# Optimization experiments

Hardware: AMD Instinct MI355X
Metric: run time of the kernel (lower is better)

Reference implementation:

```python
import jax, jax.numpy as jnp
import numpy as np

N = 50000        # total nodes
E = 800000       # edges (before self-loops)
G = 512          # graphs in batch
F_IN = 300       # num_node_features
H = 4            # heads
C = 64           # graph_hidden_channels (per head)
HC = H * C       # 256
NHID = 300
NOUT = 512
NEG_SLOPE = 0.2


def setup_inputs() -> dict:
    key = jax.random.key(0)
    ks = jax.random.split(key, 20)
    x = jax.random.normal(ks[0], (N, F_IN), dtype=jnp.float32)
    edge_index = jax.random.randint(ks[1], (2, E), 0, N, dtype=jnp.int32)
    batch = jnp.sort(jax.random.randint(ks[2], (N,), 0, G, dtype=jnp.int32))

    def lin(k, fan_in, shape):
        s = 1.0 / np.sqrt(fan_in)
        return jax.random.uniform(k, shape, jnp.float32, -s, s)

    params = {
        'W1': lin(ks[3], F_IN, (F_IN, HC)), 'a1s': lin(ks[4], C, (H, C)),
        'a1d': lin(ks[5], C, (H, C)), 'b1': jnp.zeros((HC,), jnp.float32),
        'W2': lin(ks[6], HC, (HC, HC)), 'a2s': lin(ks[7], C, (H, C)),
        'a2d': lin(ks[8], C, (H, C)), 'b2': jnp.zeros((HC,), jnp.float32),
        'W3': lin(ks[9], HC, (HC, HC)), 'a3s': lin(ks[10], C, (H, C)),
        'a3d': lin(ks[11], C, (H, C)), 'b3': jnp.zeros((HC,), jnp.float32),
        'Wm1': lin(ks[12], HC, (HC, NHID)), 'bm1': lin(ks[13], HC, (NHID,)),
        'Wm2': lin(ks[14], NHID, (NHID, NOUT)), 'bm2': lin(ks[15], NHID, (NOUT,)),
    }
    return dict(x=x, edge_index=edge_index, batch=batch, **params)


def gat_conv(x, src, dst, W, a_s, a_d, b):
    # x: [N, Fin] -> h: [N, H, C]
    h = (x @ W).reshape(N, H, C)
    al_s = jnp.sum(h * a_s, axis=-1)   # [N, H]
    al_d = jnp.sum(h * a_d, axis=-1)   # [N, H]
    e = jax.nn.leaky_relu(al_s[src] + al_d[dst], NEG_SLOPE)  # [Etot, H]
    # segment softmax over incoming edges per destination node
    m = jax.ops.segment_max(e, dst, num_segments=N)          # [N, H]
    m = jnp.where(jnp.isfinite(m), m, 0.0)
    ex = jnp.exp(e - m[dst])
    s = jax.ops.segment_sum(ex, dst, num_segments=N)
    alpha = ex / (s[dst] + 1e-16)                            # [Etot, H]
    out = jax.ops.segment_sum(alpha[:, :, None] * h[src], dst, num_segments=N)
    return out.reshape(N, HC) + b


def reference(x, edge_index, batch, W1, a1s, a1d, b1, W2, a2s, a2d, b2,
              W3, a3s, a3d, b3, Wm1, bm1, Wm2, bm2):
    loops = jnp.arange(N, dtype=edge_index.dtype)
    src = jnp.concatenate([edge_index[0], loops])
    dst = jnp.concatenate([edge_index[1], loops])

    h = jax.nn.relu(gat_conv(x, src, dst, W1, a1s, a1d, b1))
    h = jax.nn.relu(gat_conv(h, src, dst, W2, a2s, a2d, b2))
    h = gat_conv(h, src, dst, W3, a3s, a3d, b3)

    # global mean pool over graphs
    sums = jax.ops.segment_sum(h, batch, num_segments=G)           # [G, HC]
    cnts = jax.ops.segment_sum(jnp.ones((N,), h.dtype), batch, num_segments=G)
    pooled = sums / jnp.maximum(cnts, 1.0)[:, None]

    z = jax.nn.relu(pooled @ Wm1 + bm1)
    return z @ Wm2 + bm2
```

## Files before the change

### kernel.cpp

```cpp
#include <hip/hip_runtime.h>
#include <hip/hip_fp16.h>
#include <hip/hip_fp8.h>
#include <cstdint>

#define N_NODES 50000
#define M_PAD   50048
#define E_EDGES 800000
#define ETOT (E_EDGES + N_NODES)
#define G_GRAPHS 512
#define FIN 300
#define K1P 320
#define HC 256
#define NHID 300
#define NOUT 512
#define NBLK 196
#define ROWB 391
#define QPX  49

typedef unsigned short u16;
typedef unsigned char  u8;
typedef __attribute__((ext_vector_type(8))) _Float16 f16x8;
typedef __attribute__((ext_vector_type(4))) float f32x4;
typedef __attribute__((ext_vector_type(2))) float f32x2;

__device__ __forceinline__ float leaky(float x){ return x > 0.f ? x : 0.2f * x; }

#if __has_builtin(__builtin_amdgcn_cvt_pk_fp8_f32) && __has_builtin(__builtin_amdgcn_cvt_pk_f32_fp8)
#define FP8_HW 1
#else
#define FP8_HW 0
#endif

__device__ __forceinline__ u8 f2fp8(float v){
#if FP8_HW
    int b = __builtin_amdgcn_cvt_pk_fp8_f32(v, v, 0, false);
    return (u8)(b & 0xff);
#else
    return (u8)__hip_cvt_float_to_fp8(v, __HIP_SATFINITE, __HIP_E4M3);
#endif
}

__device__ __forceinline__ f32x4 fp8x4tof(unsigned u){
#if FP8_HW
    f32x2 lo = __builtin_amdgcn_cvt_pk_f32_fp8(u, false);
    f32x2 hi = __builtin_amdgcn_cvt_pk_f32_fp8(u, true);
    return (f32x4){lo.x, lo.y, hi.x, hi.y};
#else
    auto d1 = [](u8 b)->float{
        __half_raw hr = __hip_cvt_fp8_to_halfraw((__hip_fp8_storage_t)b, __HIP_E4M3);
        return __half2float(*reinterpret_cast<__half*>(&hr));
    };
    return (f32x4){d1((u8)(u & 0xff)), d1((u8)((u >> 8) & 0xff)),
                   d1((u8)((u >> 16) & 0xff)), d1((u8)((u >> 24) & 0xff))};
#endif
}

__device__ __forceinline__ unsigned packh2(float a, float b){
    __half2 h = __floats2half2_rn(a, b);
    return *reinterpret_cast<unsigned*>(&h);
}
__device__ __forceinline__ float2 unpackh2(unsigned u){
    __half2 h = *reinterpret_cast<__half2*>(&u);
    return __half22float2(h);
}

__global__ void zero_i32(int* __restrict__ p, int n){
    int i = blockIdx.x * blockDim.x + threadIdx.x;
    if (i < n) p[i] = 0;
}

__global__ void hist_kernel(const int* __restrict__ ei, int* __restrict__ counts){
    int i = blockIdx.x * blockDim.x + threadIdx.x;
    if (i >= ETOT) return;
    int d = (i < E_EDGES) ? ei[E_EDGES + i] : (i - E_EDGES);
    atomicAdd(&counts[d], 1);
}


__global__ __launch_bounds__(256) void bsum_kernel(const int* __restrict__ counts,
                                                   int* __restrict__ bsum){
    int b = blockIdx.x, t = threadIdx.x;
    int i = b * 256 + t;
    int v = (i < N_NODES) ? counts[i] : 0;
    #pragma unroll
    for (int o = 32; o >= 1; o >>= 1) v += __shfl_xor(v, o, 64);
    __shared__ int ws[4];
    if ((t & 63) == 0) ws[t >> 6] = v;
    __syncthreads();
    if (t == 0) bsum[b] = ws[0] + ws[1] + ws[2] + ws[3];
}

__global__ __launch_bounds__(256) void bscan_kernel(const int* __restrict__ bsum,
                                                    int* __restrict__ boff,
                                                    int* __restrict__ rs){
    int t = threadIdx.x;
    int v = (t < NBLK) ? bsum[t] : 0;
    __shared__ int sd[256];
    sd[t] = v;
    __syncthreads();
    for (int off = 1; off < 256; off <<= 1){
        int u = (t >= off) ? sd[t - off] : 0;
        __syncthreads();
        sd[t] += u;
        __syncthreads();
    }
    if (t < NBLK) boff[t] = sd[t] - v;
    if (t == 0) rs[N_NODES] = ETOT;
}

__global__ __launch_bounds__(256) void offsets_kernel(const int* __restrict__ counts,
                                                      const int* __restrict__ boff,
                                                      int* __restrict__ rs,
                                                      int* __restrict__ cursor){
    int b = blockIdx.x, t = threadIdx.x;
    int i = b * 256 + t;
    int v = (i < N_NODES) ? counts[i] : 0;
    __shared__ int sd[256];
    sd[t] = v;
    __syncthreads();
    for (int off = 1; off < 256; off <<= 1){
        int u = (t >= off) ? sd[t - off] : 0;
        __syncthreads();
        sd[t] += u;
        __syncthreads();
    }
    if (i < N_NODES){
        int o = boff[b] + sd[t] - v;
        rs[i] = o; cursor[i] = o;
    }
}

__global__ void scatter_kernel(const int* __restrict__ ei, int* __restrict__ cursor,
                               int* __restrict__ csr_src){
    int i = blockIdx.x * blockDim.x + threadIdx.x;
    if (i >= ETOT) return;
    int s, d;
    if (i < E_EDGES){ s = ei[i]; d = ei[E_EDGES + i]; }
    else            { s = d = i - E_EDGES; }
    int pos = atomicAdd(&cursor[d], 1);
    csr_src[pos] = s;
}


__global__ void conv_x_kernel(const float* __restrict__ x, __half* __restrict__ xf){
    int row = blockIdx.x, t = threadIdx.x;
    float v = 0.f;
    if (row < N_NODES && t < FIN) v = x[(size_t)row * FIN + t];
    xf[(size_t)row * K1P + t] = __float2half(v);
}

__global__ void conv_w_kernel(const float* __restrict__ W, __half* __restrict__ wf,
                              int K, int Kp){
    int col = blockIdx.x, k = threadIdx.x;
    float v = (k < K) ? W[(size_t)k * HC + col] : 0.f;
    wf[(size_t)col * Kp + k] = __float2half(v);
}

__global__ void pad_h_kernel(__half* __restrict__ hf){
    int row = N_NODES + blockIdx.x;
    int t = threadIdx.x;
    hf[(size_t)row * HC + t] = __float2half(0.f);
}

__global__ __launch_bounds__(256) void gemm_fp16(const __half* __restrict__ A,
                                                 const __half* __restrict__ Bt,
                                                 u8* __restrict__ Cq,
                                                 int Kp, int Mvalid){
    const int wgid = blockIdx.x;
    const int x    = wgid & 7, i = wgid >> 3;
    const int y    = x * QPX + (i >> 1);
    if (y >= ROWB) return;
    const int cx   = i & 1;
    const int col0 = cx * 128;
    const int row0 = y * 128;

    __shared__ u16 smem[16384];
    const int t    = threadIdx.x;
    const int lane = t & 63;
    const int w    = t >> 6;
    const int fr   = lane & 15, fq = lane >> 4;

    const int rA0 = t >> 2, sA0 = t & 3;

    auto aoff = [](int db, int row, int slot)->int{
        return db * 4096 + row * 32 + ((slot ^ ((row >> 1) & 3)) * 8);
    };
    auto boff = [](int db, int row, int slot)->int{
        return 8192 + db * 4096 + row * 32 + ((slot ^ ((row >> 1) & 3)) * 8);
    };

    f32x4 acc[2][8];
    #pragma unroll
    for (int m = 0; m < 2; ++m)
        #pragma unroll
        for (int n = 0; n < 8; ++n) acc[m][n] = (f32x4){0.f, 0.f, 0.f, 0.f};

    const int nt = Kp >> 5;
    int4 va0, va1, vb0, vb1;

    auto stage_load = [&](int kt){
        const int k0 = kt * 32;
        va0 = *(const int4*)(A  + (size_t)(row0 + rA0)      * Kp + k0 + sA0 * 8);
        va1 = *(const int4*)(A  + (size_t)(row0 + rA0 + 64) * Kp + k0 + sA0 * 8);
        vb0 = *(const int4*)(Bt + (size_t)(col0 + rA0)      * Kp + k0 + sA0 * 8);
        vb1 = *(const int4*)(Bt + (size_t)(col0 + rA0 + 64) * Kp + k0 + sA0 * 8);
    };
    auto stage_write = [&](int db){
        *(int4*)&smem[aoff(db, rA0,      sA0)] = va0;
        *(int4*)&smem[aoff(db, rA0 + 64, sA0)] = va1;
        *(int4*)&smem[boff(db, rA0,      sA0)] = vb0;
        *(int4*)&smem[boff(db, rA0 + 64, sA0)] = vb1;
    };

    stage_load(0); stage_write(0);
    __syncthreads();

    for (int kt = 0; kt < nt; ++kt){
        const int db = kt & 1;
        if (kt + 1 < nt) stage_load(kt + 1);

        f16x8 af[2], bf[8];
        #pragma unroll
        for (int m = 0; m < 2; ++m){
            int row = w * 32 + m * 16 + fr;
            af[m] = *(const f16x8*)&smem[aoff(db, row, fq)];
        }
        #pragma unroll
        for (int n = 0; n < 8; ++n){
            int col = n * 16 + fr;
            bf[n] = *(const f16x8*)&smem[boff(db, col, fq)];
        }
        #pragma unroll
        for (int m = 0; m < 2; ++m)
            #pragma unroll
            for (int n = 0; n < 8; ++n)
                acc[m][n] = __builtin_amdgcn_mfma_f32_16x16x32_f16(af[m], bf[n], acc[m][n], 0, 0, 0);

        if (kt + 1 < nt) stage_write(db ^ 1);
        __syncthreads();
    }

    #pragma unroll
    for (int m = 0; m < 2; ++m){
        int rowb = row0 + w * 32 + m * 16 + fq * 4;
        #pragma unroll
        for (int r = 0; r < 4; ++r){
            int row = rowb + r;
            if (row < Mvalid){
                #pragma unroll
                for (int n = 0; n < 8; ++n)
                    Cq[(size_t)row * HC + col0 + n * 16 + fr] = f2fp8(acc[m][n][r]);
            }
        }
    }
}

__global__ __launch_bounds__(256) void al_kernel(const u8* __restrict__ htq,
                                                 const float* __restrict__ a_s,
                                                 const float* __restrict__ a_d,
                                                 float* __restrict__ als,
                                                 float* __restrict__ ald){
    int wave = threadIdx.x >> 6, lane = threadIdx.x & 63;
    int n = blockIdx.x * 4 + wave;
    if (n >= N_NODES) return;
    const unsigned u = *(const unsigned*)(htq + (size_t)n * HC + 4 * lane);
    f32x4 f = fp8x4tof(u);
    const float4 as4 = *(const float4*)(a_s + 4 * lane);
    const float4 ad4 = *(const float4*)(a_d + 4 * lane);
    float ps = f.x * as4.x + f.y * as4.y + f.z * as4.z + f.w * as4.w;
    float pd = f.x * ad4.x + f.y * ad4.y + f.z * ad4.z + f.w * ad4.w;
    #pragma unroll
    for (int o = 8; o >= 1; o >>= 1){
        ps += __shfl_xor(ps, o, 64);
        pd += __shfl_xor(pd, o, 64);
    }
    if ((lane & 15) == 0){
        als[n * 4 + (lane >> 4)] = ps;
        ald[n * 4 + (lane >> 4)] = pd;
    }
}

__global__ __launch_bounds__(256) void aggregate_kernel(const u8* __restrict__ htq,
                                                        const float* __restrict__ als,
                                                        const float* __restrict__ ald,
                                                        const int* __restrict__ rs,
                                                        const int* __restrict__ csr,
                                                        const float* __restrict__ bias,
                                                        __half* __restrict__ hf,
                                                        int do_relu){
    int wave = threadIdx.x >> 6, lane = threadIdx.x & 63;
    int n = blockIdx.x * 4 + wave;
    if (n >= N_NODES) return;
    const int s0 = rs[n], s1 = rs[n + 1];
    const int deg = s1 - s0;
    const int hsel = lane >> 4;
    const float4 adv = *(const float4*)(ald + (size_t)n * 4);
    const float ad0 = adv.x, ad1 = adv.y, ad2 = adv.z, ad3 = adv.w;

    float4 acc = {0.f, 0.f, 0.f, 0.f};
    float sm0 = 0.f, sm1 = 0.f, sm2 = 0.f, sm3 = 0.f;

    if (deg <= 64){
        const int i = s0 + lane;
        int s = 0;
        float ex0 = 0.f, ex1 = 0.f, ex2 = 0.f, ex3 = 0.f;
        if (i < s1){
            s = csr[i];
            float4 a = *(const float4*)(als + (size_t)s * 4);
            ex0 = __expf(leaky(a.x + ad0));
            ex1 = __expf(leaky(a.y + ad1));
            ex2 = __expf(leaky(a.z + ad2));
            ex3 = __expf(leaky(a.w + ad3));
        }
        sm0 = ex0; sm1 = ex1; sm2 = ex2; sm3 = ex3;
        const unsigned p01 = packh2(ex0, ex1);
        const unsigned p23 = packh2(ex2, ex3);
        const bool loH = (hsel < 2);
        const bool evH = ((hsel & 1) == 0);

        const int dp = (deg + 7) & ~7;
        for (int j = 0; j < dp; j += 8){
            int sj[8]; float aw[8];
            #pragma unroll
            for (int k = 0; k < 8; ++k){
                const int jj = j + k;
                sj[k] = __shfl(s, jj, 64);
                unsigned q01 = __shfl(p01, jj, 64);
                unsigned q23 = __shfl(p23, jj, 64);
                float2 f2 = unpackh2(loH ? q01 : q23);
                aw[k] = evH ? f2.x : f2.y;
            }
            unsigned u[8];
            #pragma unroll
            for (int k = 0; k < 8; ++k)
                u[k] = *(const unsigned*)(htq + (size_t)sj[k] * HC + 4 * lane);
            #pragma unroll
            for (int k = 0; k < 8; ++k){
                f32x4 f = fp8x4tof(u[k]);
                acc.x += aw[k] * f.x; acc.y += aw[k] * f.y;
                acc.z += aw[k] * f.z; acc.w += aw[k] * f.w;
            }
        }
    } else {
        for (int base = s0; base < s1; base += 64){
            const int i = base + lane;
            int s = 0;
            float ex0 = 0.f, ex1 = 0.f, ex2 = 0.f, ex3 = 0.f;
            if (i < s1){
                s = csr[i];
                float4 a = *(const float4*)(als + (size_t)s * 4);
                ex0 = __expf(leaky(a.x + ad0));
                ex1 = __expf(leaky(a.y + ad1));
                ex2 = __expf(leaky(a.z + ad2));
                ex3 = __expf(leaky(a.w + ad3));
            }
            sm0 += ex0; sm1 += ex1; sm2 += ex2; sm3 += ex3;
            const int cnt = min(64, s1 - base);
            for (int j = 0; j < cnt; ++j){
                int   sj = __shfl(s,   j, 64);
                float a0 = __shfl(ex0, j, 64);
                float a1 = __shfl(ex1, j, 64);
                float a2 = __shfl(ex2, j, 64);
                float a3 = __shfl(ex3, j, 64);
                float x0 = (hsel == 0) ? a0 : a1;
                float x1 = (hsel == 2) ? a2 : a3;
                float aw = (hsel < 2) ? x0 : x1;
                unsigned u = *(const unsigned*)(htq + (size_t)sj * HC + 4 * lane);
                f32x4 f = fp8x4tof(u);
                acc.x += aw * f.x; acc.y += aw * f.y;
                acc.z += aw * f.z; acc.w += aw * f.w;
            }
        }
    }

    #pragma unroll
    for (int o = 32; o >= 1; o >>= 1){
        sm0 += __shfl_xor(sm0, o, 64);
        sm1 += __shfl_xor(sm1, o, 64);
        sm2 += __shfl_xor(sm2, o, 64);
        sm3 += __shfl_xor(sm3, o, 64);
    }
    float x0 = (hsel == 0) ? sm0 : sm1;
    float x1 = (hsel == 2) ? sm2 : sm3;
    const float inv = 1.f / (((hsel < 2) ? x0 : x1) + 1e-16f);

    const float4 bv = *(const float4*)(bias + 4 * lane);
    float v0 = acc.x * inv + bv.x;
    float v1 = acc.y * inv + bv.y;
    float v2 = acc.z * inv + bv.z;
    float v3 = acc.w * inv + bv.w;
    if (do_relu){
        v0 = fmaxf(v0, 0.f); v1 = fmaxf(v1, 0.f);
        v2 = fmaxf(v2, 0.f); v3 = fmaxf(v3, 0.f);
    }
    ushort4 p;
    p.x = __half_as_ushort(__float2half(v0));
    p.y = __half_as_ushort(__float2half(v1));
    p.z = __half_as_ushort(__float2half(v2));
    p.w = __half_as_ushort(__float2half(v3));
    *(ushort4*)((u16*)hf + (size_t)n * HC + 4 * lane) = p;
}

__global__ void gstart_kernel(const int* __restrict__ batch, int* __restrict__ gstart){
    int g = blockIdx.x * blockDim.x + threadIdx.x;
    if (g > G_GRAPHS) return;
    int lo = 0, hi = N_NODES;
    while (lo < hi){
        int mid = (lo + hi) >> 1;
        if (batch[mid] < g) lo = mid + 1; else hi = mid;
    }
    gstart[g] = lo;
}

__global__ __launch_bounds__(256) void pool_kernel(const __half* __restrict__ h,
                                                   const int* __restrict__ gstart,
                                                   float* __restrict__ pooled){
    int g = blockIdx.x, t = threadIdx.x;
    int s0 = gstart[g], s1 = gstart[g + 1];
    float sum = 0.f;
    for (int n = s0; n < s1; ++n) sum += __half2float(h[(size_t)n * HC + t]);
    pooled[g * HC + t] = sum / fmaxf((float)(s1 - s0), 1.f);
}

__global__ void mlp1_kernel(const float* __restrict__ pooled, const float* __restrict__ Wm1,
                            const float* __restrict__ bm1, float* __restrict__ z){
    int g = blockIdx.x, j = threadIdx.x;
    if (j >= NHID) return;
    float acc = bm1[j];
    for (int k = 0; k < HC; ++k) acc += pooled[g * HC + k] * Wm1[(size_t)k * NHID + j];
    z[g * NHID + j] = fmaxf(acc, 0.f);
}

__global__ void mlp2_kernel(const float* __restrict__ z, const float* __restrict__ Wm2,
                            const float* __restrict__ bm2, float* __restrict__ out){
    int g = blockIdx.x, j = threadIdx.x;
    float acc = bm2[j];
    for (int k = 0; k < NHID; ++k) acc += z[g * NHID + k] * Wm2[(size_t)k * NOUT + j];
    out[g * NOUT + j] = acc;
}

extern "C" void kernel_launch(void* const* d_in, const int* in_sizes, int n_in,
                              void* d_out, int out_size, void* d_ws, size_t ws_size,
                              hipStream_t stream){
    const float* x    = (const float*)d_in[0];
    const int*   ei   = (const int*)  d_in[1];
    const int*   batch= (const int*)  d_in[2];
    const float* W1   = (const float*)d_in[3];
    const float* a1s  = (const float*)d_in[4];
    const float* a1d  = (const float*)d_in[5];
    const float* b1   = (const float*)d_in[6];
    const float* W2   = (const float*)d_in[7];
    const float* a2s  = (const float*)d_in[8];
    const float* a2d  = (const float*)d_in[9];
    const float* b2   = (const float*)d_in[10];
    const float* W3   = (const float*)d_in[11];
    const float* a3s  = (const float*)d_in[12];
    const float* a3d  = (const float*)d_in[13];
    const float* b3   = (const float*)d_in[14];
    const float* Wm1  = (const float*)d_in[15];
    const float* bm1  = (const float*)d_in[16];
    const float* Wm2  = (const float*)d_in[17];
    const float* bm2  = (const float*)d_in[18];
    float* out = (float*)d_out;

    char* ws = (char*)d_ws;
    size_t off = 0;
    auto alloc = [&](size_t bytes)->char*{
        char* p = ws + off;
        off = (off + bytes + 255) & ~(size_t)255;
        return p;
    };
    __half* xf    = (__half*)alloc((size_t)M_PAD * K1P * 2);
    __half* hf    = (__half*)alloc((size_t)M_PAD * HC * 2);
    u8*     htq   = (u8*)   alloc((size_t)N_NODES * HC);
    __half* hout  = xf;
    __half* wt1   = (__half*)alloc((size_t)HC * K1P * 2);
    __half* wt2   = (__half*)alloc((size_t)HC * HC * 2);
    __half* wt3   = (__half*)alloc((size_t)HC * HC * 2);
    float* als    = (float*)alloc((size_t)N_NODES * 4 * 4);
    float* ald    = (float*)alloc((size_t)N_NODES * 4 * 4);
    int*   counts = (int*)  alloc((size_t)N_NODES * 4);
    int*   rs     = (int*)  alloc((size_t)(N_NODES + 1) * 4);
    int*   cursor = (int*)  alloc((size_t)N_NODES * 4);
    int*   csr    = (int*)  alloc((size_t)ETOT * 4);
    int*   bsum   = (int*)  alloc(256 * 4);
    int*   boffs  = (int*)  alloc(256 * 4);
    int*   gstart = (int*)  alloc((size_t)(G_GRAPHS + 1) * 4);
    float* pooled = (float*)alloc((size_t)G_GRAPHS * HC * 4);
    float* zbuf   = (float*)alloc((size_t)G_GRAPHS * NHID * 4);

    conv_x_kernel<<<M_PAD, K1P, 0, stream>>>(x, xf);
    conv_w_kernel<<<HC, K1P, 0, stream>>>(W1, wt1, FIN, K1P);
    conv_w_kernel<<<HC, HC, 0, stream>>>(W2, wt2, HC, HC);
    conv_w_kernel<<<HC, HC, 0, stream>>>(W3, wt3, HC, HC);
    pad_h_kernel<<<M_PAD - N_NODES, HC, 0, stream>>>(hf);

    zero_i32<<<(N_NODES + 255) / 256, 256, 0, stream>>>(counts, N_NODES);
    hist_kernel<<<(ETOT + 255) / 256, 256, 0, stream>>>(ei, counts);
    bsum_kernel<<<NBLK, 256, 0, stream>>>(counts, bsum);
    bscan_kernel<<<1, 256, 0, stream>>>(bsum, boffs, rs);
    offsets_kernel<<<NBLK, 256, 0, stream>>>(counts, boffs, rs, cursor);
    scatter_kernel<<<(ETOT + 255) / 256, 256, 0, stream>>>(ei, cursor, csr);
    gstart_kernel<<<3, 256, 0, stream>>>(batch, gstart);

    const int GG = 8 * 98;

    gemm_fp16<<<GG, 256, 0, stream>>>(xf, wt1, htq, K1P, N_NODES);
    al_kernel<<<(N_NODES + 3) / 4, 256, 0, stream>>>(htq, a1s, a1d, als, ald);
    aggregate_kernel<<<(N_NODES + 3) / 4, 256, 0, stream>>>(htq, als, ald, rs, csr,
                                                            b1, hf, 1);
    gemm_fp16<<<GG, 256, 0, stream>>>(hf, wt2, htq, HC, N_NODES);
    al_kernel<<<(N_NODES + 3) / 4, 256, 0, stream>>>(htq, a2s, a2d, als, ald);
    aggregate_kernel<<<(N_NODES + 3) / 4, 256, 0, stream>>>(htq, als, ald, rs, csr,
                                                            b2, hf, 1);
    gemm_fp16<<<GG, 256, 0, stream>>>(hf, wt3, htq, HC, N_NODES);
    al_kernel<<<(N_NODES + 3) / 4, 256, 0, stream>>>(htq, a3s, a3d, als, ald);
    aggregate_kernel<<<(N_NODES + 3) / 4, 256, 0, stream>>>(htq, als, ald, rs, csr,
                                                            b3, hout, 0);

    pool_kernel<<<G_GRAPHS, 256, 0, stream>>>(hout, gstart, pooled);
    mlp1_kernel<<<G_GRAPHS, 320, 0, stream>>>(pooled, Wm1, bm1, zbuf);
    mlp2_kernel<<<G_GRAPHS, 512, 0, stream>>>(zbuf, Wm2, bm2, out);
}
```

Baseline: 415.0 us.

## Partition histogram and scatter atomics by destination range per XCD

Hist and scatter kernels now run 8*128 blocks. Each block handles a chunk of edges but only acts on destinations in the node range owned by its XCD (blockIdx & 7). The aim is to keep the atomic counters and cursors local to one XCD's L2, avoiding cross-die atomic traffic. In exchange, every edge index is read eight times, and the code assumes round-robin block-to-XCD dispatch.

```diff
diff --git a/kernel.cpp b/kernel.cpp
--- a/kernel.cpp
+++ b/kernel.cpp
@@ -16,6 +16,9 @@
 #define NBLK 196
 #define ROWB 391
 #define QPX  49
+#define DRANGE 6250
+#define NCHUNK 128
+#define CHUNK_E ((ETOT + NCHUNK - 1) / NCHUNK)
 
 typedef unsigned short u16;
 typedef unsigned char  u8;
@@ -69,11 +72,33 @@
     if (i < n) p[i] = 0;
 }
 
-__global__ void hist_kernel(const int* __restrict__ ei, int* __restrict__ counts){
-    int i = blockIdx.x * blockDim.x + threadIdx.x;
-    if (i >= ETOT) return;
-    int d = (i < E_EDGES) ? ei[E_EDGES + i] : (i - E_EDGES);
-    atomicAdd(&counts[d], 1);
+__global__ __launch_bounds__(256) void hist_kernel(const int* __restrict__ ei,
+                                                   int* __restrict__ counts){
+    const int xcd = blockIdx.x & 7, chunk = blockIdx.x >> 3;
+    const int lo = xcd * DRANGE, hi = lo + DRANGE;
+    const int e0 = chunk * CHUNK_E;
+    const int e1 = min(e0 + CHUNK_E, ETOT);
+    for (int i = e0 + threadIdx.x; i < e1; i += 256){
+        int d = (i < E_EDGES) ? ei[E_EDGES + i] : (i - E_EDGES);
+        if (d >= lo && d < hi) atomicAdd(&counts[d], 1);
+    }
+}
+
+__global__ __launch_bounds__(256) void scatter_kernel(const int* __restrict__ ei,
+                                                      int* __restrict__ cursor,
+                                                      int* __restrict__ csr_src){
+    const int xcd = blockIdx.x & 7, chunk = blockIdx.x >> 3;
+    const int lo = xcd * DRANGE, hi = lo + DRANGE;
+    const int e0 = chunk * CHUNK_E;
+    const int e1 = min(e0 + CHUNK_E, ETOT);
+    for (int i = e0 + threadIdx.x; i < e1; i += 256){
+        int d = (i < E_EDGES) ? ei[E_EDGES + i] : (i - E_EDGES);
+        if (d >= lo && d < hi){
+            int s = (i < E_EDGES) ? ei[i] : (i - E_EDGES);
+            int pos = atomicAdd(&cursor[d], 1);
+            csr_src[pos] = s;
+        }
+    }
 }
 
 
@@ -128,17 +153,6 @@
         int o = boff[b] + sd[t] - v;
         rs[i] = o; cursor[i] = o;
     }
-}
-
-__global__ void scatter_kernel(const int* __restrict__ ei, int* __restrict__ cursor,
-                               int* __restrict__ csr_src){
-    int i = blockIdx.x * blockDim.x + threadIdx.x;
-    if (i >= ETOT) return;
-    int s, d;
-    if (i < E_EDGES){ s = ei[i]; d = ei[E_EDGES + i]; }
-    else            { s = d = i - E_EDGES; }
-    int pos = atomicAdd(&cursor[d], 1);
-    csr_src[pos] = s;
 }
 
 
@@ -496,11 +510,11 @@
     pad_h_kernel<<<M_PAD - N_NODES, HC, 0, stream>>>(hf);
 
     zero_i32<<<(N_NODES + 255) / 256, 256, 0, stream>>>(counts, N_NODES);
-    hist_kernel<<<(ETOT + 255) / 256, 256, 0, stream>>>(ei, counts);
+    hist_kernel<<<8 * NCHUNK, 256, 0, stream>>>(ei, counts);
     bsum_kernel<<<NBLK, 256, 0, stream>>>(counts, bsum);
     bscan_kernel<<<1, 256, 0, stream>>>(bsum, boffs, rs);
     offsets_kernel<<<NBLK, 256, 0, stream>>>(counts, boffs, rs, cursor);
-    scatter_kernel<<<(ETOT + 255) / 256, 256, 0, stream>>>(ei, cursor, csr);
+    scatter_kernel<<<8 * NCHUNK, 256, 0, stream>>>(ei, cursor, csr);
     gstart_kernel<<<3, 256, 0, stream>>>(batch, gstart);
 
     const int GG = 8 * 98;
```

Result: faster. 402.8 us (-2.9%).
